# Kernel tuning notes

Measured on AMD Instinct MI355X. Metric: run time of the kernel, lower is better.

The kernel has to match this reference:

```python
import jax, jax.numpy as jnp
import numpy as np

NUM_MASHUP = 50000
NUM_API = 50000
NUM_DOMAIN = 500
MC = 768   # mashup_embed_channels
AC = 768   # api_embed_channels
DC = 768   # domain_embed_channels
FEAT = 128 # feature_dim
BETA = 0.5
NLAYERS = 3
E = 1600000  # bipartite invocations (one direction)
BATCH = 1024


def setup_inputs() -> dict:
    key = jax.random.key(0)
    ks = jax.random.split(key, 16)
    s = 0.02
    return {
        "x": jax.random.normal(ks[0], (BATCH, MC), dtype=jnp.float32),
        "mashup_embed": jax.random.normal(ks[1], (NUM_MASHUP, MC), dtype=jnp.float32),
        "domain_embed": jax.random.normal(ks[2], (NUM_DOMAIN, DC), dtype=jnp.float32),
        "api_embed": jax.random.normal(ks[3], (NUM_API, AC), dtype=jnp.float32),
        "W_sde": jax.random.normal(ks[4], (MC, FEAT), dtype=jnp.float32) * s,
        "b_sde": jnp.zeros((FEAT,), jnp.float32),
        "W_val": jax.random.normal(ks[5], (DC, FEAT), dtype=jnp.float32) * s,
        "b_val": jnp.zeros((FEAT,), jnp.float32),
        "W_key": jax.random.normal(ks[6], (DC, FEAT), dtype=jnp.float32) * s,
        "b_key": jnp.zeros((FEAT,), jnp.float32),
        "W_sie": jax.random.normal(ks[7], (AC, FEAT), dtype=jnp.float32) * s,
        "b_sie": jnp.zeros((FEAT,), jnp.float32),
        "edge_src": jax.random.randint(ks[8], (E,), 0, NUM_MASHUP, dtype=jnp.int32),
        "edge_dst": jax.random.randint(ks[9], (E,), 0, NUM_API, dtype=jnp.int32),
    }


def _sig_lin(h, W, b):
    # nn.Linear + Sigmoid
    return jax.nn.sigmoid(h @ W + b)


def _lightgcn(emb, row, col, num_nodes, num_layers):
    # PyG LightGCN.get_embedding: mean of layer-0..L embeddings with
    # symmetric gcn_norm propagation over the bipartite graph.
    ones = jnp.ones(row.shape, emb.dtype)
    deg = jax.ops.segment_sum(ones, row, num_segments=num_nodes)
    dinv = jnp.where(deg > 0, jax.lax.rsqrt(deg), 0.0)
    norm = dinv[row] * dinv[col]  # [2E]
    alpha = 1.0 / (num_layers + 1)
    x_l = emb
    out = emb * alpha
    for _ in range(num_layers):
        # message x[row]*norm scattered to col (graph is symmetric)
        x_l = jax.ops.segment_sum(x_l[row] * norm[:, None], col, num_segments=num_nodes)
        out = out + x_l * alpha
    return out


def reference(x, mashup_embed, domain_embed, api_embed,
              W_sde, b_sde, W_val, b_val, W_key, b_key, W_sie, b_sie,
              edge_src, edge_dst):
    batch = x.shape[0]
    # --- attention pooling over domain embeddings (SDE branch) ---
    v_mi = _sig_lin(x, W_sde, b_sde)                 # [B, F]
    v_value = _sig_lin(domain_embed, W_val, b_val)   # [D, F]
    v_key = _sig_lin(domain_embed, W_key, b_key)     # [D, F]
    al = v_mi @ v_key.T                              # [B, D]
    alpha = al / jnp.sum(al, axis=1, keepdims=True)  # normalized (no softmax)
    s_m = alpha @ v_value                            # [B, F]
    z_m = (1.0 - BETA) * s_m + BETA * v_mi           # [B, F]
    # --- LightGCN propagation over mashup-api bipartite graph ---
    v_m = _sig_lin(mashup_embed, W_sde, b_sde)       # [Nm, F]
    v_s = _sig_lin(api_embed, W_sie, b_sie)          # [Na, F]
    emb = jnp.concatenate([v_m, v_s], axis=0)        # [N, F]
    num_nodes = NUM_MASHUP + NUM_API
    src = edge_src.astype(jnp.int32)
    dst = edge_dst.astype(jnp.int32) + NUM_MASHUP
    row = jnp.concatenate([src, dst])                # [2E] symmetric edges
    col = jnp.concatenate([dst, src])
    out = _lightgcn(emb, row, col, num_nodes, NLAYERS)
    O = out[NUM_MASHUP:]                             # [Na, F]
    # --- dot-product scoring ---
    pred = z_m @ O.T                                 # [B, Na]
    return pred
```

## Files before the change

kernel.cpp:

```cpp
#include <hip/hip_runtime.h>
#include <hip/hip_bf16.h>
#include <cstddef>
#include <cstdint>

#define NM 50000
#define NA 50000
#define ND 500
#define FEAT 128
#define KDIM 768
#define BATCH 1024
#define NEDGE 1600000
#define MD 128

#define NBIN 196
#define CAP 10240
#define F1B 400
#define F1E (NEDGE / F1B)

#define PB128 391
#define PKT   24

typedef __bf16 bf16_t;
typedef bf16_t bf16x8 __attribute__((ext_vector_type(8)));
typedef bf16_t bf16x4 __attribute__((ext_vector_type(4)));
typedef float f32x4 __attribute__((ext_vector_type(4)));
typedef float f32x2 __attribute__((ext_vector_type(2)));
typedef unsigned short u16;
typedef unsigned char u8;

__device__ __forceinline__ float sigf(float x) { return 1.0f / (1.0f + __expf(-x)); }

__device__ __forceinline__ float4 dec4fp8(uint32_t w) {
  f32x2 lo = __builtin_amdgcn_cvt_pk_f32_fp8(w, false);
  f32x2 hi = __builtin_amdgcn_cvt_pk_f32_fp8(w, true);
  return make_float4(lo[0], lo[1], hi[0], hi[1]);
}
__device__ __forceinline__ u8 enc1fp8(float a) {
  return (u8)(__builtin_amdgcn_cvt_pk_fp8_f32(a, a, 0, false) & 0xff);
}

__device__ __forceinline__ void gll16(const void* g, void* l) {
  __builtin_amdgcn_global_load_lds(
      (const __attribute__((address_space(1))) unsigned int*)g,
      (__attribute__((address_space(3))) unsigned int*)l, 16, 0, 0);
}

__global__ __launch_bounds__(256) void fill_bin_wt(
    const int* __restrict__ src, const int* __restrict__ dst,
    int* __restrict__ bcur, uint32_t* __restrict__ rec,
    const float* __restrict__ W0, const float* __restrict__ W1,
    const float* __restrict__ W2, const float* __restrict__ W3,
    bf16_t* __restrict__ T0, bf16_t* __restrict__ T1,
    bf16_t* __restrict__ T2, bf16_t* __restrict__ T3)
{
  __shared__ uint32_t edg[F1E];
  __shared__ int hist[2 * NBIN];
  __shared__ int base[2 * NBIN];
  if (blockIdx.x >= F1B) {
    const int b = blockIdx.x - F1B;
    const float* W = (b < 128) ? W0 : (b < 256) ? W1 : (b < 384) ? W2 : W3;
    bf16_t* T      = (b < 128) ? T0 : (b < 256) ? T1 : (b < 384) ? T2 : T3;
    int c = b & 127;
    for (int k = threadIdx.x; k < KDIM; k += 256)
      T[(size_t)c * KDIM + k] = (bf16_t)W[(size_t)k * FEAT + c];
    return;
  }
  const int tid = threadIdx.x;
  for (int i = tid; i < 2 * NBIN; i += 256) hist[i] = 0;
  __syncthreads();
  const int e0 = blockIdx.x * F1E;
  for (int i = tid; i < F1E; i += 256) {
    int s = __builtin_nontemporal_load(&src[e0 + i]);
    int d = __builtin_nontemporal_load(&dst[e0 + i]);
    edg[i] = ((uint32_t)s << 16) | (uint32_t)d;
    atomicAdd(&hist[s >> 8], 1);
    atomicAdd(&hist[NBIN + (d >> 8)], 1);
  }
  __syncthreads();
  for (int i = tid; i < 2 * NBIN; i += 256) {
    int c = hist[i];
    base[i] = c ? atomicAdd(&bcur[i], c) : 0;
    hist[i] = 0;
  }
  __syncthreads();
  for (int i = tid; i < F1E; i += 256) {
    uint32_t e = edg[i];
    int s = (int)(e >> 16), d = (int)(e & 0xffffu);
    int bm = s >> 8, ba = NBIN + (d >> 8);
    int rm = base[bm] + atomicAdd(&hist[bm], 1);
    int ra = base[ba] + atomicAdd(&hist[ba], 1);
    if (rm < CAP) rec[(size_t)bm * CAP + rm] = e;
    if (ra < CAP) rec[(size_t)ba * CAP + ra] = ((uint32_t)d << 16) | (uint32_t)s;
  }
}

__global__ __launch_bounds__(256) void fill_ell2(
    const uint32_t* __restrict__ rec, const int* __restrict__ bcur,
    u16* __restrict__ adjm, u16* __restrict__ adja,
    int* __restrict__ cnt_m, int* __restrict__ cnt_a,
    float* __restrict__ dm, float* __restrict__ da)
{
  __shared__ int cnt256[256];
  const int g = blockIdx.x;
  const int side = g >= NBIN;
  const int bin = side ? g - NBIN : g;
  u16* adj = side ? adja : adjm;
  int* cnt = side ? cnt_a : cnt_m;
  float* dv = side ? da : dm;
  cnt256[threadIdx.x] = 0;
  __syncthreads();
  int n = bcur[g]; if (n > CAP) n = CAP;
  const uint32_t* rb = rec + (size_t)g * CAP;
  for (int i = threadIdx.x; i < n; i += 256) {
    uint32_t r = rb[i];
    int node = (int)(r >> 16);
    int rk = atomicAdd(&cnt256[node & 255], 1);
    if (rk < MD) adj[(size_t)node * MD + rk] = (u16)(r & 0xffffu);
  }
  __syncthreads();
  int node = bin * 256 + threadIdx.x;
  if (node < NM) {
    int c = cnt256[threadIdx.x];
    cnt[node] = c;
    dv[node] = c > 0 ? rsqrtf((float)c) : 0.f;
  }
}

template<int OM>
__device__ __forceinline__ void proj8(
    char* smraw,
    const float* __restrict__ A, const bf16_t* __restrict__ Wt,
    const float* __restrict__ bias, void* __restrict__ Cout, int M, int rowBase,
    const float* __restrict__ rowscale, bf16_t* __restrict__ C2)
{
  const int tid = threadIdx.x;
  const int lane = tid & 63;
  const int wid = tid >> 6;

  int arow = rowBase + wid * 16 + (lane & 15); if (arow > M - 1) arow = M - 1;
  const float*  asrc = A  + (size_t)arow * KDIM + ((lane >> 4) * 8);
  const bf16_t* bsrc = Wt + (size_t)(wid * 16 + (lane & 15)) * KDIM + ((lane >> 4) * 8);

  f32x4 acc[8];
  #pragma unroll
  for (int n = 0; n < 8; ++n) acc[n] = (f32x4){0.f, 0.f, 0.f, 0.f};

  auto stage = [&](int kt, int s) {
    const int k0 = kt * 32;
    char* base = smraw + s * 24576;
    gll16(asrc + k0,     base + wid * 2048);
    gll16(asrc + k0 + 4, base + wid * 2048 + 1024);
    gll16(bsrc + k0,     base + 16384 + wid * 1024);
  };

  stage(0, 0);

  for (int kt = 0; kt < PKT; ++kt) {
    if (kt + 1 < PKT) {
      stage(kt + 1, (kt + 1) & 1);
      asm volatile("s_waitcnt vmcnt(3)" ::: "memory");
    } else {
      asm volatile("s_waitcnt vmcnt(0)" ::: "memory");
    }
    __builtin_amdgcn_s_barrier();
    asm volatile("" ::: "memory");

    const char* bb = smraw + (kt & 1) * 24576;
    f32x4 lo = *(const f32x4*)(bb + wid * 2048 + lane * 16);
    f32x4 hi = *(const f32x4*)(bb + wid * 2048 + 1024 + lane * 16);
    bf16x8 a;
    a[0] = (bf16_t)lo[0]; a[1] = (bf16_t)lo[1]; a[2] = (bf16_t)lo[2]; a[3] = (bf16_t)lo[3];
    a[4] = (bf16_t)hi[0]; a[5] = (bf16_t)hi[1]; a[6] = (bf16_t)hi[2]; a[7] = (bf16_t)hi[3];
    #pragma unroll
    for (int n = 0; n < 8; ++n) {
      bf16x8 bfr = *(const bf16x8*)(bb + 16384 + n * 1024 + lane * 16);
      acc[n] = __builtin_amdgcn_mfma_f32_16x16x32_bf16(a, bfr, acc[n], 0, 0, 0);
    }

    asm volatile("" ::: "memory");
    __builtin_amdgcn_s_barrier();
  }

  const int r0 = (lane >> 4) * 4, cc = lane & 15;
  #pragma unroll
  for (int n = 0; n < 8; ++n) {
    int col = n * 16 + cc;
    float bb = bias[col];
    #pragma unroll
    for (int r = 0; r < 4; ++r) {
      int row = rowBase + wid * 16 + r0 + r;
      if (row < M) {
        float v = sigf(acc[n][r] + bb);
        float sc = rowscale ? rowscale[row] : 1.0f;
        if constexpr (OM == 2)
          ((u8*)Cout)[(size_t)row * FEAT + col] = enc1fp8(v * sc);
        else
          ((float*)Cout)[(size_t)row * FEAT + col] = v * sc;
        if (C2) C2[(size_t)row * FEAT + col] = (bf16_t)(0.25f * v);
      }
    }
  }
}

__global__ __launch_bounds__(512, 4) void proj_all(
    const float* __restrict__ mashup, const float* __restrict__ api,
    const float* __restrict__ x, const float* __restrict__ domain,
    const bf16_t* __restrict__ wt0, const bf16_t* __restrict__ wt1,
    const bf16_t* __restrict__ wt2, const bf16_t* __restrict__ wt3,
    const float* __restrict__ bsde, const float* __restrict__ bkey,
    const float* __restrict__ bval, const float* __restrict__ bsie,
    u8* __restrict__ M0y8, u8* __restrict__ y0a8,
    float* __restrict__ vmi, float* __restrict__ vkey, float* __restrict__ vval,
    const float* __restrict__ dm, const float* __restrict__ da,
    bf16_t* __restrict__ outA)
{
  __shared__ alignas(16) char smem[2 * 24576];
  const int b = blockIdx.x;
  if (b < PB128)
    proj8<2>(smem, mashup, wt0, bsde, M0y8, NM, b * 128, dm, nullptr);
  else if (b < 2 * PB128)
    proj8<2>(smem, api, wt3, bsie, y0a8, NA, (b - PB128) * 128, da, outA);
  else if (b < 2 * PB128 + 8)
    proj8<0>(smem, x, wt0, bsde, vmi, BATCH, (b - 2 * PB128) * 128, nullptr, nullptr);
  else if (b < 2 * PB128 + 12)
    proj8<0>(smem, domain, wt1, bkey, vkey, ND, (b - 2 * PB128 - 8) * 128, nullptr, nullptr);
  else
    proj8<0>(smem, domain, wt2, bval, vval, ND, (b - 2 * PB128 - 12) * 128, nullptr, nullptr);
}

__global__ __launch_bounds__(256) void attn_kernel(
    const float* __restrict__ vmi, const float* __restrict__ vkey,
    const float* __restrict__ vval, bf16_t* __restrict__ zm)
{
  const int i = blockIdx.x;
  const int tid = threadIdx.x;
  __shared__ float vs[FEAT];
  __shared__ float al[ND];
  __shared__ float red[4];
  __shared__ float ps[256];
  __shared__ float totS;
  if (tid < FEAT) vs[tid] = vmi[(size_t)i * FEAT + tid];
  __syncthreads();
  float part = 0.f;
  for (int j = tid; j < ND; j += 256) {
    const float* kr = vkey + (size_t)j * FEAT;
    float dot = 0.f;
    #pragma unroll 8
    for (int k = 0; k < FEAT; k += 4) {
      float4 kv = *(const float4*)(kr + k);
      dot += vs[k] * kv.x + vs[k + 1] * kv.y + vs[k + 2] * kv.z + vs[k + 3] * kv.w;
    }
    al[j] = dot;
    part += dot;
  }
  #pragma unroll
  for (int o = 32; o > 0; o >>= 1) part += __shfl_down(part, o, 64);
  if ((tid & 63) == 0) red[tid >> 6] = part;
  __syncthreads();
  if (tid == 0) totS = red[0] + red[1] + red[2] + red[3];
  const int f = tid & 127, h = tid >> 7;
  float s = 0.f;
  const float* vv = vval + (size_t)h * 250 * FEAT + f;
  #pragma unroll 5
  for (int j = 0; j < 250; ++j) s += al[h * 250 + j] * vv[(size_t)j * FEAT];
  ps[tid] = s;
  __syncthreads();
  if (tid < FEAT) {
    float z = 0.5f * ((ps[tid] + ps[128 + tid]) / totS + vs[tid]);
    zm[(size_t)i * FEAT + tid] = (bf16_t)z;
  }
}

__device__ __forceinline__ float4 gatherF8(const uint32_t* __restrict__ base32,
                                           const u16* __restrict__ row,
                                           int n, int half)
{
  float4 acc = make_float4(0.f, 0.f, 0.f, 0.f);
  int j = half;
  while (j + 14 < n) {
    int u[8];
    #pragma unroll
    for (int q = 0; q < 8; ++q) u[q] = row[j + 2 * q];
    uint32_t w[8];
    #pragma unroll
    for (int q = 0; q < 8; ++q) w[q] = base32[(size_t)u[q] * 32];
    #pragma unroll
    for (int q = 0; q < 8; ++q) {
      float4 v = dec4fp8(w[q]);
      acc.x += v.x; acc.y += v.y; acc.z += v.z; acc.w += v.w;
    }
    j += 16;
  }
  while (j < n) {
    float4 v = dec4fp8(base32[(size_t)row[j] * 32]);
    acc.x += v.x; acc.y += v.y; acc.z += v.z; acc.w += v.w;
    j += 2;
  }
  return acc;
}

#define REDUCE_HALVES(acc)                    \
  acc.x += __shfl_xor(acc.x, 32);             \
  acc.y += __shfl_xor(acc.y, 32);             \
  acc.z += __shfl_xor(acc.z, 32);             \
  acc.w += __shfl_xor(acc.w, 32);

__global__ __launch_bounds__(256) void prop_p1(
    const uint32_t* __restrict__ M0y8, const uint32_t* __restrict__ y0a8,
    uint32_t* __restrict__ y01a8,
    const u16* __restrict__ adja, const int* __restrict__ cnt_a,
    const float* __restrict__ da)
{
  const int a = blockIdx.x * 4 + (threadIdx.x >> 6);
  const int lane = threadIdx.x & 63;
  const int half = lane >> 5, sl = lane & 31;
  int n = cnt_a[a]; if (n > MD) n = MD;
  float4 acc = gatherF8(M0y8 + sl, adja + (size_t)a * MD, n, half);
  REDUCE_HALVES(acc)
  if (half == 0) {
    const float d = da[a];
    const float s2 = d * d;
    float4 b = dec4fp8(y0a8[(size_t)a * 32 + sl]);
    uint32_t o = __builtin_amdgcn_cvt_pk_fp8_f32(b.x + s2 * acc.x, b.y + s2 * acc.y, 0, false);
    o = __builtin_amdgcn_cvt_pk_fp8_f32(b.z + s2 * acc.z, b.w + s2 * acc.w, o, true);
    y01a8[(size_t)a * 32 + sl] = o;
  }
}

__global__ __launch_bounds__(256) void prop_p2(
    const uint32_t* __restrict__ y01a8, const uint32_t* __restrict__ M0y8,
    uint32_t* __restrict__ Sy8,
    const u16* __restrict__ adjm, const int* __restrict__ cnt_m,
    const float* __restrict__ dm)
{
  const int m = blockIdx.x * 4 + (threadIdx.x >> 6);
  const int lane = threadIdx.x & 63;
  const int half = lane >> 5, sl = lane & 31;
  int n = cnt_m[m]; if (n > MD) n = MD;
  float4 acc = gatherF8(y01a8 + sl, adjm + (size_t)m * MD, n, half);
  REDUCE_HALVES(acc)
  if (half == 0) {
    const float d = dm[m];
    const float s2 = d * d;
    float4 b = dec4fp8(M0y8[(size_t)m * 32 + sl]);
    uint32_t o = __builtin_amdgcn_cvt_pk_fp8_f32(b.x + s2 * acc.x, b.y + s2 * acc.y, 0, false);
    o = __builtin_amdgcn_cvt_pk_fp8_f32(b.z + s2 * acc.z, b.w + s2 * acc.w, o, true);
    Sy8[(size_t)m * 32 + sl] = o;
  }
}

__global__ __launch_bounds__(256) void prop_p3(
    const uint32_t* __restrict__ Sy8, const bf16_t* __restrict__ outA,
    bf16_t* __restrict__ Obf,
    const u16* __restrict__ adja, const int* __restrict__ cnt_a,
    const float* __restrict__ da)
{
  const int a = blockIdx.x * 4 + (threadIdx.x >> 6);
  const int lane = threadIdx.x & 63;
  const int half = lane >> 5, sl = lane & 31;
  int n = cnt_a[a]; if (n > MD) n = MD;
  float4 acc = gatherF8(Sy8 + sl, adja + (size_t)a * MD, n, half);
  REDUCE_HALVES(acc)
  if (half == 0) {
    const float q = 0.25f * da[a];
    bf16x4 pv = *(const bf16x4*)(outA + (size_t)a * FEAT + 4 * sl);
    bf16x4 o;
    o[0] = (bf16_t)((float)pv[0] + q * acc.x);
    o[1] = (bf16_t)((float)pv[1] + q * acc.y);
    o[2] = (bf16_t)((float)pv[2] + q * acc.z);
    o[3] = (bf16_t)((float)pv[3] + q * acc.w);
    *(bf16x4*)(Obf + (size_t)a * FEAT + 4 * sl) = o;
  }
}

__global__ __launch_bounds__(256) void pred_mfma(
    const bf16_t* __restrict__ Z, const bf16_t* __restrict__ O,
    float* __restrict__ out)
{
  const int lane = threadIdx.x & 63;
  const int wid = threadIdx.x >> 6;
  const int nBase = blockIdx.x * 256 + wid * 64;
  const int cc = lane & 15;
  const int kOff = (lane >> 4) * 8;

  bf16x8 b[4][4];
  #pragma unroll
  for (int n = 0; n < 4; ++n) {
    int c = nBase + n * 16 + cc;
    if (c > NA - 1) c = NA - 1;
    #pragma unroll
    for (int kk = 0; kk < 4; ++kk)
      b[n][kk] = *(const bf16x8*)(O + (size_t)c * FEAT + kk * 32 + kOff);
  }

  const int r0 = (lane >> 4) * 4;
  #pragma unroll
  for (int it = 0; it < 4; ++it) {
    const int iBase = blockIdx.y * 256 + it * 64;
    f32x4 acc[4][4];
    #pragma unroll
    for (int m = 0; m < 4; ++m)
      #pragma unroll
      for (int n = 0; n < 4; ++n)
        acc[m][n] = (f32x4){0.f, 0.f, 0.f, 0.f};

    #pragma unroll
    for (int kk = 0; kk < 4; ++kk) {
      bf16x8 a[4];
      #pragma unroll
      for (int m = 0; m < 4; ++m)
        a[m] = *(const bf16x8*)(Z + (size_t)(iBase + cc + m * 16) * FEAT + kk * 32 + kOff);
      #pragma unroll
      for (int m = 0; m < 4; ++m)
        #pragma unroll
        for (int n = 0; n < 4; ++n)
          acc[m][n] = __builtin_amdgcn_mfma_f32_16x16x32_bf16(a[m], b[n][kk], acc[m][n], 0, 0, 0);
    }

    #pragma unroll
    for (int n = 0; n < 4; ++n) {
      int col = nBase + n * 16 + cc;
      if (col < NA) {
        #pragma unroll
        for (int m = 0; m < 4; ++m) {
          #pragma unroll
          for (int r = 0; r < 4; ++r) {
            int row = iBase + m * 16 + r0 + r;
            __builtin_nontemporal_store(acc[m][n][r], &out[(size_t)row * NA + col]);
          }
        }
      }
    }
  }
}

static inline char* alignup(char* p, size_t a) {
  return (char*)(((uintptr_t)p + a - 1) & ~(uintptr_t)(a - 1));
}

extern "C" void kernel_launch(void* const* d_in, const int* in_sizes, int n_in,
                              void* d_out, int out_size, void* d_ws, size_t ws_size,
                              hipStream_t stream) {
  const float* x      = (const float*)d_in[0];
  const float* mashup = (const float*)d_in[1];
  const float* domain = (const float*)d_in[2];
  const float* api    = (const float*)d_in[3];
  const float* Wsde   = (const float*)d_in[4];
  const float* bsde   = (const float*)d_in[5];
  const float* Wval   = (const float*)d_in[6];
  const float* bval   = (const float*)d_in[7];
  const float* Wkey   = (const float*)d_in[8];
  const float* bkey   = (const float*)d_in[9];
  const float* Wsie   = (const float*)d_in[10];
  const float* bsie   = (const float*)d_in[11];
  const int* esrc     = (const int*)d_in[12];
  const int* edst     = (const int*)d_in[13];
  float* out = (float*)d_out;

  char* p = (char*)d_ws;
  u8*     M0y8  = (u8*)p; p += (size_t)NM * FEAT;
  u8*     y0a8  = (u8*)p; p += (size_t)NA * FEAT;
  u8*     y01a8 = (u8*)p; p += (size_t)NA * FEAT;
  u8*     Sy8   = (u8*)p; p += (size_t)NM * FEAT;
  bf16_t* outA  = (bf16_t*)p; p += (size_t)NA * FEAT * 2;
  bf16_t* Obf   = (bf16_t*)p; p += (size_t)NA * FEAT * 2;
  u16*    adjm  = (u16*)p;    p += (size_t)NM * MD * 2;
  u16*    adja  = (u16*)p;    p += (size_t)NA * MD * 2;
  float*  vmi   = (float*)p;  p += (size_t)BATCH * FEAT * 4;
  float*  vkey  = (float*)p;  p += (size_t)ND * FEAT * 4;
  float*  vval  = (float*)p;  p += (size_t)ND * FEAT * 4;
  bf16_t* zm    = (bf16_t*)p; p += (size_t)BATCH * FEAT * 2;
  int* cnt_m = (int*)p; p += (size_t)NM * 4;
  int* cnt_a = (int*)p; p += (size_t)NA * 4;
  float* dm  = (float*)p; p += (size_t)NM * 4;
  float* da  = (float*)p; p += (size_t)NA * 4;
  int* bcur  = (int*)p; p += 512 * 4;
  p = alignup(p, 16);
  bf16_t* wt0 = (bf16_t*)p; p += (size_t)FEAT * KDIM * 2;
  bf16_t* wt1 = (bf16_t*)p; p += (size_t)FEAT * KDIM * 2;
  bf16_t* wt2 = (bf16_t*)p; p += (size_t)FEAT * KDIM * 2;
  bf16_t* wt3 = (bf16_t*)p; p += (size_t)FEAT * KDIM * 2;
  uint32_t* rec = (uint32_t*)M0y8;

  hipMemsetAsync(bcur, 0, 512 * sizeof(int), stream);

  fill_bin_wt<<<F1B + 512, 256, 0, stream>>>(esrc, edst, bcur, rec,
                                             Wsde, Wkey, Wval, Wsie,
                                             wt0, wt1, wt2, wt3);
  fill_ell2<<<2 * NBIN, 256, 0, stream>>>(rec, bcur, adjm, adja,
                                          cnt_m, cnt_a, dm, da);

  proj_all<<<2 * PB128 + 16, 512, 0, stream>>>(
      mashup, api, x, domain, wt0, wt1, wt2, wt3,
      bsde, bkey, bval, bsie, M0y8, y0a8, vmi, vkey, vval, dm, da, outA);

  attn_kernel<<<BATCH, 256, 0, stream>>>(vmi, vkey, vval, zm);

  prop_p1<<<NA / 4, 256, 0, stream>>>((const uint32_t*)M0y8, (const uint32_t*)y0a8,
                                      (uint32_t*)y01a8, adja, cnt_a, da);
  prop_p2<<<NM / 4, 256, 0, stream>>>((const uint32_t*)y01a8, (const uint32_t*)M0y8,
                                      (uint32_t*)Sy8, adjm, cnt_m, dm);
  prop_p3<<<NA / 4, 256, 0, stream>>>((const uint32_t*)Sy8, outA, Obf,
                                      adja, cnt_a, da);

  pred_mfma<<<dim3((NA + 255) / 256, BATCH / 256), 256, 0, stream>>>(zm, Obf, out);
}
```

Baseline: 402.4 us.

## Pre-swizzle weights into MFMA fragment layout and drop block-wide LDS staging

Weights are transposed into a fragment-ordered layout at prep time, so each lane reads its B operand for every MFMA straight from global memory (through cache) without LDS. A rows are loaded into registers with software prefetch, converted to bf16, and passed through a small per-wave LDS scratch to reach MFMA layout. This removes the block-wide barriers and the large double-buffered LDS tile. The cost is that every wave now re-fetches the weight fragments from global or L2, and there is a write-then-read through LDS within a wave with no explicit wave-level sync.

Result: slower. 415.4 us (+3.2%).

```diff
diff --git a/kernel.cpp b/kernel.cpp
--- a/kernel.cpp
+++ b/kernel.cpp
@@ -39,12 +39,6 @@
   return (u8)(__builtin_amdgcn_cvt_pk_fp8_f32(a, a, 0, false) & 0xff);
 }
 
-__device__ __forceinline__ void gll16(const void* g, void* l) {
-  __builtin_amdgcn_global_load_lds(
-      (const __attribute__((address_space(1))) unsigned int*)g,
-      (__attribute__((address_space(3))) unsigned int*)l, 16, 0, 0);
-}
-
 __global__ __launch_bounds__(256) void fill_bin_wt(
     const int* __restrict__ src, const int* __restrict__ dst,
     int* __restrict__ bcur, uint32_t* __restrict__ rec,
@@ -61,8 +55,11 @@
     const float* W = (b < 128) ? W0 : (b < 256) ? W1 : (b < 384) ? W2 : W3;
     bf16_t* T      = (b < 128) ? T0 : (b < 256) ? T1 : (b < 384) ? T2 : T3;
     int c = b & 127;
-    for (int k = threadIdx.x; k < KDIM; k += 256)
-      T[(size_t)c * KDIM + k] = (bf16_t)W[(size_t)k * FEAT + c];
+    for (int k = threadIdx.x; k < KDIM; k += 256) {
+      int kt = k >> 5, kq = (k >> 3) & 3, j = k & 7;
+      size_t g = ((size_t)(c >> 4) * PKT + kt) * 64 + (kq * 16 + (c & 15));
+      T[g * 8 + j] = (bf16_t)W[(size_t)k * FEAT + c];
+    }
     return;
   }
   const int tid = threadIdx.x;
@@ -129,56 +126,53 @@
 template<int OM>
 __device__ __forceinline__ void proj8(
     char* smraw,
-    const float* __restrict__ A, const bf16_t* __restrict__ Wt,
+    const float* __restrict__ A, const bf16_t* __restrict__ Wf,
     const float* __restrict__ bias, void* __restrict__ Cout, int M, int rowBase,
     const float* __restrict__ rowscale, bf16_t* __restrict__ C2)
 {
   const int tid = threadIdx.x;
   const int lane = tid & 63;
   const int wid = tid >> 6;
-
-  int arow = rowBase + wid * 16 + (lane & 15); if (arow > M - 1) arow = M - 1;
-  const float*  asrc = A  + (size_t)arow * KDIM + ((lane >> 4) * 8);
-  const bf16_t* bsrc = Wt + (size_t)(wid * 16 + (lane & 15)) * KDIM + ((lane >> 4) * 8);
+  char* lb = smraw + wid * 2560;
+
+  int r0g = rowBase + wid * 16 + (lane >> 3);
+  int r1g = r0g + 8;
+  if (r0g > M - 1) r0g = M - 1;
+  if (r1g > M - 1) r1g = M - 1;
+  const float* ap0 = A + (size_t)r0g * KDIM + (lane & 7) * 4;
+  const float* ap1 = A + (size_t)r1g * KDIM + (lane & 7) * 4;
 
   f32x4 acc[8];
   #pragma unroll
   for (int n = 0; n < 8; ++n) acc[n] = (f32x4){0.f, 0.f, 0.f, 0.f};
 
-  auto stage = [&](int kt, int s) {
-    const int k0 = kt * 32;
-    char* base = smraw + s * 24576;
-    gll16(asrc + k0,     base + wid * 2048);
-    gll16(asrc + k0 + 4, base + wid * 2048 + 1024);
-    gll16(bsrc + k0,     base + 16384 + wid * 1024);
-  };
-
-  stage(0, 0);
+  const int wb0 = (lane >> 3) * 80 + (lane & 7) * 8;
+  const int wb1 = ((lane >> 3) + 8) * 80 + (lane & 7) * 8;
+  const int rdOff = (lane & 15) * 80 + (lane >> 4) * 16;
+
+  float4 a0 = *(const float4*)ap0;
+  float4 a1 = *(const float4*)ap1;
 
   for (int kt = 0; kt < PKT; ++kt) {
+    float4 n0, n1;
     if (kt + 1 < PKT) {
-      stage(kt + 1, (kt + 1) & 1);
-      asm volatile("s_waitcnt vmcnt(3)" ::: "memory");
-    } else {
-      asm volatile("s_waitcnt vmcnt(0)" ::: "memory");
-    }
-    __builtin_amdgcn_s_barrier();
-    asm volatile("" ::: "memory");
-
-    const char* bb = smraw + (kt & 1) * 24576;
-    f32x4 lo = *(const f32x4*)(bb + wid * 2048 + lane * 16);
-    f32x4 hi = *(const f32x4*)(bb + wid * 2048 + 1024 + lane * 16);
-    bf16x8 a;
-    a[0] = (bf16_t)lo[0]; a[1] = (bf16_t)lo[1]; a[2] = (bf16_t)lo[2]; a[3] = (bf16_t)lo[3];
-    a[4] = (bf16_t)hi[0]; a[5] = (bf16_t)hi[1]; a[6] = (bf16_t)hi[2]; a[7] = (bf16_t)hi[3];
+      n0 = *(const float4*)(ap0 + (kt + 1) * 32);
+      n1 = *(const float4*)(ap1 + (kt + 1) * 32);
+    }
+    char* sb = lb + (kt & 1) * 1280;
+    bf16x4 w0, w1;
+    w0[0] = (bf16_t)a0.x; w0[1] = (bf16_t)a0.y; w0[2] = (bf16_t)a0.z; w0[3] = (bf16_t)a0.w;
+    w1[0] = (bf16_t)a1.x; w1[1] = (bf16_t)a1.y; w1[2] = (bf16_t)a1.z; w1[3] = (bf16_t)a1.w;
+    *(bf16x4*)(sb + wb0) = w0;
+    *(bf16x4*)(sb + wb1) = w1;
+    bf16x8 a = *(const bf16x8*)(sb + rdOff);
+    const bf16_t* bp = Wf + ((size_t)kt * 64 + lane) * 8;
     #pragma unroll
     for (int n = 0; n < 8; ++n) {
-      bf16x8 bfr = *(const bf16x8*)(bb + 16384 + n * 1024 + lane * 16);
+      bf16x8 bfr = *(const bf16x8*)(bp + (size_t)n * PKT * 64 * 8);
       acc[n] = __builtin_amdgcn_mfma_f32_16x16x32_bf16(a, bfr, acc[n], 0, 0, 0);
     }
-
-    asm volatile("" ::: "memory");
-    __builtin_amdgcn_s_barrier();
+    a0 = n0; a1 = n1;
   }
 
   const int r0 = (lane >> 4) * 4, cc = lane & 15;
@@ -214,7 +208,7 @@
     const float* __restrict__ dm, const float* __restrict__ da,
     bf16_t* __restrict__ outA)
 {
-  __shared__ alignas(16) char smem[2 * 24576];
+  __shared__ alignas(16) char smem[8 * 2560];
   const int b = blockIdx.x;
   if (b < PB128)
     proj8<2>(smem, mashup, wt0, bsde, M0y8, NM, b * 128, dm, nullptr);
```

## Swizzle projection A-tile LDS layout and fuse attention with first propagation pass

Applied to the files above, without the earlier changes.

The projection kernel's fp32 A-tile staging is reorganized so each lane loads a row-chunk with an XOR swizzle, and the LDS read offsets are recomputed to match. This aims to cut LDS bank conflicts when the MFMA A fragments are read. Separately, the attention kernel and the first LightGCN propagation pass are merged into one launch with block-index dispatch. This removes one kernel launch and lets the two independent workloads run concurrently. The merged kernel reserves the attention shared memory for every block, which may lower occupancy for the gather blocks.

New measurement: 379.1 us. 1.06x faster.

```diff
diff --git a/kernel.cpp b/kernel.cpp
--- a/kernel.cpp
+++ b/kernel.cpp
@@ -137,8 +137,12 @@
   const int lane = tid & 63;
   const int wid = tid >> 6;
 
-  int arow = rowBase + wid * 16 + (lane & 15); if (arow > M - 1) arow = M - 1;
-  const float*  asrc = A  + (size_t)arow * KDIM + ((lane >> 4) * 8);
+  const int srow = lane >> 3;
+  const int schunk = (lane & 7) ^ srow;
+  int g0 = rowBase + wid * 16 + srow;     if (g0 > M - 1) g0 = M - 1;
+  int g1 = rowBase + wid * 16 + 8 + srow; if (g1 > M - 1) g1 = M - 1;
+  const float* asrc0 = A + (size_t)g0 * KDIM + schunk * 4;
+  const float* asrc1 = A + (size_t)g1 * KDIM + schunk * 4;
   const bf16_t* bsrc = Wt + (size_t)(wid * 16 + (lane & 15)) * KDIM + ((lane >> 4) * 8);
 
   f32x4 acc[8];
@@ -148,12 +152,18 @@
   auto stage = [&](int kt, int s) {
     const int k0 = kt * 32;
     char* base = smraw + s * 24576;
-    gll16(asrc + k0,     base + wid * 2048);
-    gll16(asrc + k0 + 4, base + wid * 2048 + 1024);
-    gll16(bsrc + k0,     base + 16384 + wid * 1024);
+    gll16(asrc0 + k0, base + wid * 2048);
+    gll16(asrc1 + k0, base + wid * 2048 + 1024);
+    gll16(bsrc + k0,  base + 16384 + wid * 1024);
   };
 
   stage(0, 0);
+
+  const int row16 = lane & 15, h = lane >> 4;
+  const int rd1 = (row16 & 7) * 128 + ((row16 >> 3) ? 1024 : 0) +
+                  ((2 * h) ^ (row16 & 7)) * 16;
+  const int rd2 = (row16 & 7) * 128 + ((row16 >> 3) ? 1024 : 0) +
+                  ((2 * h + 1) ^ (row16 & 7)) * 16;
 
   for (int kt = 0; kt < PKT; ++kt) {
     if (kt + 1 < PKT) {
@@ -166,8 +176,8 @@
     asm volatile("" ::: "memory");
 
     const char* bb = smraw + (kt & 1) * 24576;
-    f32x4 lo = *(const f32x4*)(bb + wid * 2048 + lane * 16);
-    f32x4 hi = *(const f32x4*)(bb + wid * 2048 + 1024 + lane * 16);
+    f32x4 lo = *(const f32x4*)(bb + wid * 2048 + rd1);
+    f32x4 hi = *(const f32x4*)(bb + wid * 2048 + rd2);
     bf16x8 a;
     a[0] = (bf16_t)lo[0]; a[1] = (bf16_t)lo[1]; a[2] = (bf16_t)lo[2]; a[3] = (bf16_t)lo[3];
     a[4] = (bf16_t)hi[0]; a[5] = (bf16_t)hi[1]; a[6] = (bf16_t)hi[2]; a[7] = (bf16_t)hi[3];
@@ -228,12 +238,67 @@
     proj8<0>(smem, domain, wt2, bval, vval, ND, (b - 2 * PB128 - 12) * 128, nullptr, nullptr);
 }
 
-__global__ __launch_bounds__(256) void attn_kernel(
+__device__ __forceinline__ float4 gatherF8(const uint32_t* __restrict__ base32,
+                                           const u16* __restrict__ row,
+                                           int n, int half)
+{
+  float4 acc = make_float4(0.f, 0.f, 0.f, 0.f);
+  int j = half;
+  while (j + 14 < n) {
+    int u[8];
+    #pragma unroll
+    for (int q = 0; q < 8; ++q) u[q] = row[j + 2 * q];
+    uint32_t w[8];
+    #pragma unroll
+    for (int q = 0; q < 8; ++q) w[q] = base32[(size_t)u[q] * 32];
+    #pragma unroll
+    for (int q = 0; q < 8; ++q) {
+      float4 v = dec4fp8(w[q]);
+      acc.x += v.x; acc.y += v.y; acc.z += v.z; acc.w += v.w;
+    }
+    j += 16;
+  }
+  while (j < n) {
+    float4 v = dec4fp8(base32[(size_t)row[j] * 32]);
+    acc.x += v.x; acc.y += v.y; acc.z += v.z; acc.w += v.w;
+    j += 2;
+  }
+  return acc;
+}
+
+#define REDUCE_HALVES(acc)                    \
+  acc.x += __shfl_xor(acc.x, 32);             \
+  acc.y += __shfl_xor(acc.y, 32);             \
+  acc.z += __shfl_xor(acc.z, 32);             \
+  acc.w += __shfl_xor(acc.w, 32);
+
+__global__ __launch_bounds__(256) void attn_p1(
     const float* __restrict__ vmi, const float* __restrict__ vkey,
-    const float* __restrict__ vval, bf16_t* __restrict__ zm)
-{
+    const float* __restrict__ vval, bf16_t* __restrict__ zm,
+    const uint32_t* __restrict__ M0y8, const uint32_t* __restrict__ y0a8,
+    uint32_t* __restrict__ y01a8,
+    const u16* __restrict__ adja, const int* __restrict__ cnt_a,
+    const float* __restrict__ da)
+{
+  const int tid = threadIdx.x;
+  if (blockIdx.x >= BATCH) {
+    const int a = (blockIdx.x - BATCH) * 4 + (tid >> 6);
+    const int lane = tid & 63;
+    const int half = lane >> 5, sl = lane & 31;
+    int n = cnt_a[a]; if (n > MD) n = MD;
+    float4 acc = gatherF8(M0y8 + sl, adja + (size_t)a * MD, n, half);
+    REDUCE_HALVES(acc)
+    if (half == 0) {
+      const float d = da[a];
+      const float s2 = d * d;
+      float4 b = dec4fp8(y0a8[(size_t)a * 32 + sl]);
+      uint32_t o = __builtin_amdgcn_cvt_pk_fp8_f32(b.x + s2 * acc.x, b.y + s2 * acc.y, 0, false);
+      o = __builtin_amdgcn_cvt_pk_fp8_f32(b.z + s2 * acc.z, b.w + s2 * acc.w, o, true);
+      y01a8[(size_t)a * 32 + sl] = o;
+    }
+    return;
+  }
   const int i = blockIdx.x;
-  const int tid = threadIdx.x;
   __shared__ float vs[FEAT];
   __shared__ float al[ND];
   __shared__ float red[4];
@@ -268,62 +333,6 @@
   if (tid < FEAT) {
     float z = 0.5f * ((ps[tid] + ps[128 + tid]) / totS + vs[tid]);
     zm[(size_t)i * FEAT + tid] = (bf16_t)z;
-  }
-}
-
-__device__ __forceinline__ float4 gatherF8(const uint32_t* __restrict__ base32,
-                                           const u16* __restrict__ row,
-                                           int n, int half)
-{
-  float4 acc = make_float4(0.f, 0.f, 0.f, 0.f);
-  int j = half;
-  while (j + 14 < n) {
-    int u[8];
-    #pragma unroll
-    for (int q = 0; q < 8; ++q) u[q] = row[j + 2 * q];
-    uint32_t w[8];
-    #pragma unroll
-    for (int q = 0; q < 8; ++q) w[q] = base32[(size_t)u[q] * 32];
-    #pragma unroll
-    for (int q = 0; q < 8; ++q) {
-      float4 v = dec4fp8(w[q]);
-      acc.x += v.x; acc.y += v.y; acc.z += v.z; acc.w += v.w;
-    }
-    j += 16;
-  }
-  while (j < n) {
-    float4 v = dec4fp8(base32[(size_t)row[j] * 32]);
-    acc.x += v.x; acc.y += v.y; acc.z += v.z; acc.w += v.w;
-    j += 2;
-  }
-  return acc;
-}
-
-#define REDUCE_HALVES(acc)                    \
-  acc.x += __shfl_xor(acc.x, 32);             \
-  acc.y += __shfl_xor(acc.y, 32);             \
-  acc.z += __shfl_xor(acc.z, 32);             \
-  acc.w += __shfl_xor(acc.w, 32);
-
-__global__ __launch_bounds__(256) void prop_p1(
-    const uint32_t* __restrict__ M0y8, const uint32_t* __restrict__ y0a8,
-    uint32_t* __restrict__ y01a8,
-    const u16* __restrict__ adja, const int* __restrict__ cnt_a,
-    const float* __restrict__ da)
-{
-  const int a = blockIdx.x * 4 + (threadIdx.x >> 6);
-  const int lane = threadIdx.x & 63;
-  const int half = lane >> 5, sl = lane & 31;
-  int n = cnt_a[a]; if (n > MD) n = MD;
-  float4 acc = gatherF8(M0y8 + sl, adja + (size_t)a * MD, n, half);
-  REDUCE_HALVES(acc)
-  if (half == 0) {
-    const float d = da[a];
-    const float s2 = d * d;
-    float4 b = dec4fp8(y0a8[(size_t)a * 32 + sl]);
-    uint32_t o = __builtin_amdgcn_cvt_pk_fp8_f32(b.x + s2 * acc.x, b.y + s2 * acc.y, 0, false);
-    o = __builtin_amdgcn_cvt_pk_fp8_f32(b.z + s2 * acc.z, b.w + s2 * acc.w, o, true);
-    y01a8[(size_t)a * 32 + sl] = o;
   }
 }
 
@@ -494,10 +503,11 @@
       mashup, api, x, domain, wt0, wt1, wt2, wt3,
       bsde, bkey, bval, bsie, M0y8, y0a8, vmi, vkey, vval, dm, da, outA);
 
-  attn_kernel<<<BATCH, 256, 0, stream>>>(vmi, vkey, vval, zm);
-
-  prop_p1<<<NA / 4, 256, 0, stream>>>((const uint32_t*)M0y8, (const uint32_t*)y0a8,
-                                      (uint32_t*)y01a8, adja, cnt_a, da);
+  attn_p1<<<BATCH + NA / 4, 256, 0, stream>>>(
+      vmi, vkey, vval, zm,
+      (const uint32_t*)M0y8, (const uint32_t*)y0a8, (uint32_t*)y01a8,
+      adja, cnt_a, da);
+
   prop_p2<<<NM / 4, 256, 0, stream>>>((const uint32_t*)y01a8, (const uint32_t*)M0y8,
                                       (uint32_t*)Sy8, adjm, cnt_m, dm);
   prop_p3<<<NA / 4, 256, 0, stream>>>((const uint32_t*)Sy8, outA, Obf,
```
